# Performance work log

Measured on AMD Instinct MI355X. Metric: run time of the kernel, lower is better.

The kernel has to match this reference:

```python
import jax, jax.numpy as jnp
import numpy as np

N_NODES = 100000


def gcn_conv(x, edge_index, W, b):
    """PyG GCNConv: h = x @ W; out = D^-1/2 (A+I) D^-1/2 h + b."""
    n = x.shape[0]
    src, dst = edge_index[0], edge_index[1]
    loop = jnp.arange(n)
    src = jnp.concatenate([src, loop])  # add self-loops
    dst = jnp.concatenate([dst, loop])
    # degree at target nodes (unit edge weights)
    deg = jax.ops.segment_sum(jnp.ones(dst.shape[0], dtype=x.dtype), dst, num_segments=n)
    dinv = jnp.where(deg > 0, jax.lax.rsqrt(deg), 0.0)
    norm = dinv[src] * dinv[dst]  # [E+n]
    h = x @ W  # [n, out]
    msg = h[src] * norm[:, None]  # gather + scale
    out = jax.ops.segment_sum(msg, dst, num_segments=n)  # scatter-add
    return out + b


def setup_inputs() -> dict:
    key = jax.random.key(0)
    k1, k2, k3, k4, k5, k6 = jax.random.split(key, 6)
    E = 3200000
    x = jax.random.normal(k1, (N_NODES, 2), dtype=jnp.float32)
    edge_index = jax.random.randint(k2, (2, E), 0, N_NODES, dtype=jnp.int64)
    W1 = jax.random.normal(k3, (2, 16), dtype=jnp.float32) * 0.5
    b1 = jax.random.normal(k4, (16,), dtype=jnp.float32) * 0.1
    W2 = jax.random.normal(k5, (16, 2), dtype=jnp.float32) * 0.25
    b2 = jax.random.normal(k6, (2,), dtype=jnp.float32) * 0.1
    return {"x": x, "edge_index": edge_index, "W1": W1, "b1": b1, "W2": W2, "b2": b2}


def reference(x, edge_index, W1, b1, W2, b2):
    h = jax.nn.relu(gcn_conv(x, edge_index, W1, b1))
    # dropout is identity at inference
    out = gcn_conv(h, edge_index, W2, b2)
    return jax.nn.log_softmax(out, axis=1)
```

## Files before the change

kernel.cpp:

```cpp
#include <hip/hip_runtime.h>
#include <math.h>


constexpr int N = 100000;
constexpr int LOGB = 6;
constexpr int BNODES = 1 << LOGB;
constexpr int K = (N + BNODES - 1) / BNODES;
constexpr int KF = 49 * 32;
constexpr int CAPF = 2560;
constexpr int NC = 49;
constexpr int CAP1 = 68608;
constexpr int BSP = 512;
constexpr int ECHUNK = 8192;
constexpr int EPT = ECHUNK / BSP;
constexpr int MAXCH = 9;

__global__ __launch_bounds__(BSP) void k_pass1(const int* __restrict__ src,
                                               const int* __restrict__ dst, int E,
                                               int* __restrict__ gfill1,
                                               int* __restrict__ slotsC) {
    __shared__ int hist[NC];
    __shared__ int base[NC];
    int t = threadIdx.x;
    if (t < NC) hist[t] = 0;
    __syncthreads();
    int s[EPT], d[EPT];
    int ebase = blockIdx.x * ECHUNK + t * EPT;
#pragma unroll
    for (int k = 0; k < EPT / 4; k++) {
        int idx = ebase + 4 * k;
        if (idx + 3 < E) {
            *(int4*)(s + 4 * k) = *(const int4*)(src + idx);
            *(int4*)(d + 4 * k) = *(const int4*)(dst + idx);
        } else {
            for (int j = 0; j < 4; j++) {
                s[4 * k + j] = (idx + j < E) ? src[idx + j] : -1;
                d[4 * k + j] = (idx + j < E) ? dst[idx + j] : -1;
            }
        }
    }
#pragma unroll
    for (int k = 0; k < EPT; k++)
        if (d[k] >= 0) atomicAdd(&hist[d[k] >> 11], 1);
    __syncthreads();
    if (t < NC) {
        int c = hist[t];
        base[t] = c ? atomicAdd(&gfill1[t], c) : 0;
        hist[t] = 0;
    }
    __syncthreads();
#pragma unroll
    for (int k = 0; k < EPT; k++) {
        if (d[k] >= 0) {
            int bin = d[k] >> 11;
            int r = atomicAdd(&hist[bin], 1);
            int pos = base[bin] + r;
            if (pos < CAP1) slotsC[bin * CAP1 + pos] = (s[k] << 11) | (d[k] & 2047);
        }
    }
}

__global__ __launch_bounds__(BSP) void k_pass2(const int* __restrict__ gfill1,
                                               const int* __restrict__ slotsC,
                                               int* __restrict__ gfillF,
                                               int* __restrict__ slotsF) {
    __shared__ int hist[32];
    __shared__ int base[32];
    int c = blockIdx.x / MAXCH;
    int j = blockIdx.x % MAXCH;
    int fill = min(gfill1[c], CAP1);
    int e0 = j * ECHUNK;
    if (e0 >= fill) return;
    int e1 = min(fill, e0 + ECHUNK);
    int t = threadIdx.x;
    if (t < 32) hist[t] = 0;
    __syncthreads();
    const int* row = slotsC + c * CAP1;
    int v[EPT];
    int ebase = e0 + t * EPT;
#pragma unroll
    for (int k = 0; k < EPT / 4; k++) {
        int idx = ebase + 4 * k;
        if (idx + 3 < e1) {
            *(int4*)(v + 4 * k) = *(const int4*)(row + idx);
        } else {
            for (int jj = 0; jj < 4; jj++) v[4 * k + jj] = (idx + jj < e1) ? row[idx + jj] : -1;
        }
    }
#pragma unroll
    for (int k = 0; k < EPT; k++)
        if (v[k] >= 0) atomicAdd(&hist[(v[k] >> 6) & 31], 1);
    __syncthreads();
    if (t < 32) {
        int cc = hist[t];
        base[t] = cc ? atomicAdd(&gfillF[c * 32 + t], cc) : 0;
        hist[t] = 0;
    }
    __syncthreads();
#pragma unroll
    for (int k = 0; k < EPT; k++) {
        if (v[k] >= 0) {
            int b = (v[k] >> 6) & 31;
            int r = atomicAdd(&hist[b], 1);
            int pos = base[b] + r;
            if (pos < CAPF)
                slotsF[(c * 32 + b) * CAPF + pos] = ((v[k] >> 11) << 6) | (v[k] & 63);
        }
    }
}

__global__ __launch_bounds__(512) void k_degree(const int* __restrict__ gfillF,
                                                const int* __restrict__ slotsF,
                                                const float* __restrict__ x,
                                                float* __restrict__ dinv,
                                                float2* __restrict__ sx) {
    __shared__ int cnt[BNODES];
    int b = blockIdx.x, t = threadIdx.x;
    if (t < BNODES) cnt[t] = 0;
    __syncthreads();
    int count = min(gfillF[b], CAPF);
    const int* row = slotsF + b * CAPF;
    int nvec = count & ~3;
    for (int j = 4 * t; j < nvec; j += 4 * 512) {
        int4 p = *(const int4*)(row + j);
        atomicAdd(&cnt[p.x & (BNODES - 1)], 1);
        atomicAdd(&cnt[p.y & (BNODES - 1)], 1);
        atomicAdd(&cnt[p.z & (BNODES - 1)], 1);
        atomicAdd(&cnt[p.w & (BNODES - 1)], 1);
    }
    for (int j = nvec + t; j < count; j += 512) atomicAdd(&cnt[row[j] & (BNODES - 1)], 1);
    __syncthreads();
    if (t < BNODES) {
        int node = b * BNODES + t;
        if (node < N) {
            float di = rsqrtf((float)(cnt[t] + 1));
            dinv[node] = di;
            float2 xv = ((const float2*)x)[node];
            sx[node] = make_float2(xv.x * di, xv.y * di);
        }
    }
}

__global__ __launch_bounds__(512) void k_agg1(const int* __restrict__ gfillF,
                                              const int* __restrict__ slotsF,
                                              const float* __restrict__ dinv,
                                              const float2* __restrict__ sx,
                                              const float* __restrict__ W1,
                                              const float* __restrict__ b1,
                                              const float* __restrict__ W2,
                                              float2* __restrict__ sz) {
    __shared__ float accX[BNODES], accY[BNODES];
    __shared__ float sW1[32], sb1[16], sW2[32];
    int t = threadIdx.x;
    if (t < 32) sW1[t] = W1[t];
    if (t >= 32 && t < 48) sb1[t - 32] = b1[t - 32];
    if (t >= 48 && t < 80) sW2[t - 48] = W2[t - 48];
    if (t < BNODES) { accX[t] = 0.f; accY[t] = 0.f; }
    __syncthreads();
    int b = blockIdx.x;
    int count = min(gfillF[b], CAPF);
    const int* row = slotsF + b * CAPF;
    int nvec = count & ~3;
    for (int j = 4 * t; j < nvec; j += 4 * 512) {
        int4 p = *(const int4*)(row + j);
        float2 v0 = sx[p.x >> LOGB], v1 = sx[p.y >> LOGB];
        float2 v2 = sx[p.z >> LOGB], v3 = sx[p.w >> LOGB];
        atomicAdd(&accX[p.x & (BNODES - 1)], v0.x);
        atomicAdd(&accY[p.x & (BNODES - 1)], v0.y);
        atomicAdd(&accX[p.y & (BNODES - 1)], v1.x);
        atomicAdd(&accY[p.y & (BNODES - 1)], v1.y);
        atomicAdd(&accX[p.z & (BNODES - 1)], v2.x);
        atomicAdd(&accY[p.z & (BNODES - 1)], v2.y);
        atomicAdd(&accX[p.w & (BNODES - 1)], v3.x);
        atomicAdd(&accY[p.w & (BNODES - 1)], v3.y);
    }
    for (int j = nvec + t; j < count; j += 512) {
        int p = row[j];
        float2 v = sx[p >> LOGB];
        atomicAdd(&accX[p & (BNODES - 1)], v.x);
        atomicAdd(&accY[p & (BNODES - 1)], v.y);
    }
    __syncthreads();
    if (t < BNODES) {
        int node = b * BNODES + t;
        if (node < N) {
            float di = dinv[node];
            float2 sv = sx[node];
            float a0 = (accX[t] + sv.x) * di;
            float a1 = (accY[t] + sv.y) * di;
            float z0 = 0.f, z1 = 0.f;
#pragma unroll
            for (int k = 0; k < 16; k++) {
                float h = fmaf(a0, sW1[k], fmaf(a1, sW1[16 + k], sb1[k]));
                h = fmaxf(h, 0.f);
                z0 = fmaf(h, sW2[2 * k + 0], z0);
                z1 = fmaf(h, sW2[2 * k + 1], z1);
            }
            sz[node] = make_float2(z0 * di, z1 * di);
        }
    }
}

__global__ __launch_bounds__(512) void k_agg2(const int* __restrict__ gfillF,
                                              const int* __restrict__ slotsF,
                                              const float* __restrict__ dinv,
                                              const float2* __restrict__ sz,
                                              const float* __restrict__ b2,
                                              float2* __restrict__ out) {
    __shared__ float accX[BNODES], accY[BNODES];
    int b = blockIdx.x, t = threadIdx.x;
    if (t < BNODES) { accX[t] = 0.f; accY[t] = 0.f; }
    __syncthreads();
    int count = min(gfillF[b], CAPF);
    const int* row = slotsF + b * CAPF;
    int nvec = count & ~3;
    for (int j = 4 * t; j < nvec; j += 4 * 512) {
        int4 p = *(const int4*)(row + j);
        float2 v0 = sz[p.x >> LOGB], v1 = sz[p.y >> LOGB];
        float2 v2 = sz[p.z >> LOGB], v3 = sz[p.w >> LOGB];
        atomicAdd(&accX[p.x & (BNODES - 1)], v0.x);
        atomicAdd(&accY[p.x & (BNODES - 1)], v0.y);
        atomicAdd(&accX[p.y & (BNODES - 1)], v1.x);
        atomicAdd(&accY[p.y & (BNODES - 1)], v1.y);
        atomicAdd(&accX[p.z & (BNODES - 1)], v2.x);
        atomicAdd(&accY[p.z & (BNODES - 1)], v2.y);
        atomicAdd(&accX[p.w & (BNODES - 1)], v3.x);
        atomicAdd(&accY[p.w & (BNODES - 1)], v3.y);
    }
    for (int j = nvec + t; j < count; j += 512) {
        int p = row[j];
        float2 v = sz[p >> LOGB];
        atomicAdd(&accX[p & (BNODES - 1)], v.x);
        atomicAdd(&accY[p & (BNODES - 1)], v.y);
    }
    __syncthreads();
    if (t < BNODES) {
        int node = b * BNODES + t;
        if (node < N) {
            float di = dinv[node];
            float2 sv = sz[node];
            float v0 = fmaf(accX[t] + sv.x, di, b2[0]);
            float v1 = fmaf(accY[t] + sv.y, di, b2[1]);
            float m = fmaxf(v0, v1);
            float lse = m + logf(expf(v0 - m) + expf(v1 - m));
            out[node] = make_float2(v0 - lse, v1 - lse);
        }
    }
}

extern "C" void kernel_launch(void* const* d_in, const int* in_sizes, int n_in,
                              void* d_out, int out_size, void* d_ws, size_t ws_size,
                              hipStream_t stream) {
    const float* x  = (const float*)d_in[0];
    const int*   ei = (const int*)d_in[1];
    const float* W1 = (const float*)d_in[2];
    const float* b1 = (const float*)d_in[3];
    const float* W2 = (const float*)d_in[4];
    const float* b2 = (const float*)d_in[5];

    const int E = in_sizes[1] / 2;
    const int* src = ei;
    const int* dst = ei + E;
    const int GP = (E + ECHUNK - 1) / ECHUNK;

    char* ws = (char*)d_ws;
    size_t off = 0;
    auto alloc = [&](size_t bytes) {
        char* p = ws + off;
        off += (bytes + 511) & ~size_t(511);
        return p;
    };
    int*    fills  = (int*)alloc((NC + KF) * sizeof(int));
    float*  dinv   = (float*)alloc(N * sizeof(float));
    float2* sx     = (float2*)alloc(N * sizeof(float2));
    float2* sz     = (float2*)alloc(N * sizeof(float2));
    int*    slotsC = (int*)alloc((size_t)NC * CAP1 * sizeof(int));
    int*    slotsF = (int*)alloc((size_t)KF * CAPF * sizeof(int));
    int* gfill1 = fills;
    int* gfillF = fills + NC;

    hipMemsetAsync(fills, 0, (NC + KF) * sizeof(int), stream);

    k_pass1<<<GP, BSP, 0, stream>>>(src, dst, E, gfill1, slotsC);
    k_pass2<<<NC * MAXCH, BSP, 0, stream>>>(gfill1, slotsC, gfillF, slotsF);
    k_degree<<<K, 512, 0, stream>>>(gfillF, slotsF, x, dinv, sx);
    k_agg1<<<K, 512, 0, stream>>>(gfillF, slotsF, dinv, sx, W1, b1, W2, sz);
    k_agg2<<<K, 512, 0, stream>>>(gfillF, slotsF, dinv, sz, b2, (float2*)d_out);
}
```

Measured before the change: 203.2 us.

## Fuse degree counting into bucket pass and batch aggregation gathers

Degree counting moves into the second bucketing pass: each block keeps a 2048-bin shared histogram and writes partial counts, which a small per-node kernel sums to produce dinv and the scaled features. This removes the separate k_degree pass over the fine-grained slot array. The aggregation kernels now use 256 threads, each loading up to 12 packed edges up front and issuing all feature gathers before the shared atomics, to raise memory-level parallelism. In exchange, the early return for empty chunks is gone, adding shared-memory init and partial-count writes for every block. The fixed 12-per-thread scheme also assumes bucket counts stay within the 2560 capacity.

```diff
diff --git a/kernel.cpp b/kernel.cpp
--- a/kernel.cpp
+++ b/kernel.cpp
@@ -63,18 +63,20 @@
 __global__ __launch_bounds__(BSP) void k_pass2(const int* __restrict__ gfill1,
                                                const int* __restrict__ slotsC,
                                                int* __restrict__ gfillF,
-                                               int* __restrict__ slotsF) {
+                                               int* __restrict__ slotsF,
+                                               int* __restrict__ cntp) {
     __shared__ int hist[32];
     __shared__ int base[32];
+    __shared__ int cnt[2048];
     int c = blockIdx.x / MAXCH;
     int j = blockIdx.x % MAXCH;
+    int t = threadIdx.x;
+    if (t < 32) hist[t] = 0;
+    for (int i = t; i < 2048; i += BSP) cnt[i] = 0;
+    __syncthreads();
     int fill = min(gfill1[c], CAP1);
     int e0 = j * ECHUNK;
-    if (e0 >= fill) return;
     int e1 = min(fill, e0 + ECHUNK);
-    int t = threadIdx.x;
-    if (t < 32) hist[t] = 0;
-    __syncthreads();
     const int* row = slotsC + c * CAP1;
     int v[EPT];
     int ebase = e0 + t * EPT;
@@ -88,8 +90,12 @@
         }
     }
 #pragma unroll
-    for (int k = 0; k < EPT; k++)
-        if (v[k] >= 0) atomicAdd(&hist[(v[k] >> 6) & 31], 1);
+    for (int k = 0; k < EPT; k++) {
+        if (v[k] >= 0) {
+            atomicAdd(&hist[(v[k] >> 6) & 31], 1);
+            atomicAdd(&cnt[v[k] & 2047], 1);
+        }
+    }
     __syncthreads();
     if (t < 32) {
         int cc = hist[t];
@@ -107,41 +113,36 @@
                 slotsF[(c * 32 + b) * CAPF + pos] = ((v[k] >> 11) << 6) | (v[k] & 63);
         }
     }
-}
-
-__global__ __launch_bounds__(512) void k_degree(const int* __restrict__ gfillF,
-                                                const int* __restrict__ slotsF,
-                                                const float* __restrict__ x,
-                                                float* __restrict__ dinv,
-                                                float2* __restrict__ sx) {
-    __shared__ int cnt[BNODES];
-    int b = blockIdx.x, t = threadIdx.x;
-    if (t < BNODES) cnt[t] = 0;
-    __syncthreads();
-    int count = min(gfillF[b], CAPF);
-    const int* row = slotsF + b * CAPF;
-    int nvec = count & ~3;
-    for (int j = 4 * t; j < nvec; j += 4 * 512) {
-        int4 p = *(const int4*)(row + j);
-        atomicAdd(&cnt[p.x & (BNODES - 1)], 1);
-        atomicAdd(&cnt[p.y & (BNODES - 1)], 1);
-        atomicAdd(&cnt[p.z & (BNODES - 1)], 1);
-        atomicAdd(&cnt[p.w & (BNODES - 1)], 1);
-    }
-    for (int j = nvec + t; j < count; j += 512) atomicAdd(&cnt[row[j] & (BNODES - 1)], 1);
-    __syncthreads();
-    if (t < BNODES) {
-        int node = b * BNODES + t;
-        if (node < N) {
-            float di = rsqrtf((float)(cnt[t] + 1));
-            dinv[node] = di;
-            float2 xv = ((const float2*)x)[node];
-            sx[node] = make_float2(xv.x * di, xv.y * di);
-        }
-    }
-}
-
-__global__ __launch_bounds__(512) void k_agg1(const int* __restrict__ gfillF,
+    int* out = cntp + (size_t)blockIdx.x * 2048;
+    *(int4*)(out + 4 * t) = *(const int4*)(cnt + 4 * t);
+}
+
+__global__ void k_node1(const int* __restrict__ cntp, const float* __restrict__ x,
+                        float* __restrict__ dinv, float2* __restrict__ sx) {
+    int i = blockIdx.x * blockDim.x + threadIdx.x;
+    if (i >= N) return;
+    int c = i >> 11, l = i & 2047;
+    const int* p = cntp + (size_t)c * MAXCH * 2048 + l;
+    int s = 0;
+#pragma unroll
+    for (int j = 0; j < MAXCH; j++) s += p[j * 2048];
+    float di = rsqrtf((float)(s + 1));
+    dinv[i] = di;
+    float2 xv = ((const float2*)x)[i];
+    sx[i] = make_float2(xv.x * di, xv.y * di);
+}
+
+__device__ __forceinline__ int4 gload(const int* __restrict__ row, int j, int cnt) {
+    if (j + 3 < cnt) return *(const int4*)(row + j);
+    int4 p = make_int4(-1, -1, -1, -1);
+    if (j + 0 < cnt) p.x = row[j + 0];
+    if (j + 1 < cnt) p.y = row[j + 1];
+    if (j + 2 < cnt) p.z = row[j + 2];
+    if (j + 3 < cnt) p.w = row[j + 3];
+    return p;
+}
+
+__global__ __launch_bounds__(256) void k_agg1(const int* __restrict__ gfillF,
                                               const int* __restrict__ slotsF,
                                               const float* __restrict__ dinv,
                                               const float2* __restrict__ sx,
@@ -159,26 +160,28 @@
     __syncthreads();
     int b = blockIdx.x;
     int count = min(gfillF[b], CAPF);
-    const int* row = slotsF + b * CAPF;
-    int nvec = count & ~3;
-    for (int j = 4 * t; j < nvec; j += 4 * 512) {
-        int4 p = *(const int4*)(row + j);
-        float2 v0 = sx[p.x >> LOGB], v1 = sx[p.y >> LOGB];
-        float2 v2 = sx[p.z >> LOGB], v3 = sx[p.w >> LOGB];
-        atomicAdd(&accX[p.x & (BNODES - 1)], v0.x);
-        atomicAdd(&accY[p.x & (BNODES - 1)], v0.y);
-        atomicAdd(&accX[p.y & (BNODES - 1)], v1.x);
-        atomicAdd(&accY[p.y & (BNODES - 1)], v1.y);
-        atomicAdd(&accX[p.z & (BNODES - 1)], v2.x);
-        atomicAdd(&accY[p.z & (BNODES - 1)], v2.y);
-        atomicAdd(&accX[p.w & (BNODES - 1)], v3.x);
-        atomicAdd(&accY[p.w & (BNODES - 1)], v3.y);
-    }
-    for (int j = nvec + t; j < count; j += 512) {
-        int p = row[j];
-        float2 v = sx[p >> LOGB];
-        atomicAdd(&accX[p & (BNODES - 1)], v.x);
-        atomicAdd(&accY[p & (BNODES - 1)], v.y);
+    const int* row = slotsF + (size_t)b * CAPF;
+    int pk[12];
+    {
+        int4 p0 = gload(row, 4 * t, count);
+        int4 p1 = gload(row, 4 * t + 1024, count);
+        int4 p2 = gload(row, 4 * t + 2048, count);
+        pk[0] = p0.x; pk[1] = p0.y; pk[2] = p0.z; pk[3] = p0.w;
+        pk[4] = p1.x; pk[5] = p1.y; pk[6] = p1.z; pk[7] = p1.w;
+        pk[8] = p2.x; pk[9] = p2.y; pk[10] = p2.z; pk[11] = p2.w;
+    }
+    float2 vv[12];
+#pragma unroll
+    for (int m = 0; m < 12; m++) {
+        int idx = (pk[m] >= 0) ? (pk[m] >> LOGB) : 0;
+        vv[m] = sx[idx];
+    }
+#pragma unroll
+    for (int m = 0; m < 12; m++) {
+        if (pk[m] >= 0) {
+            atomicAdd(&accX[pk[m] & (BNODES - 1)], vv[m].x);
+            atomicAdd(&accY[pk[m] & (BNODES - 1)], vv[m].y);
+        }
     }
     __syncthreads();
     if (t < BNODES) {
@@ -201,7 +204,7 @@
     }
 }
 
-__global__ __launch_bounds__(512) void k_agg2(const int* __restrict__ gfillF,
+__global__ __launch_bounds__(256) void k_agg2(const int* __restrict__ gfillF,
                                               const int* __restrict__ slotsF,
                                               const float* __restrict__ dinv,
                                               const float2* __restrict__ sz,
@@ -212,26 +215,28 @@
     if (t < BNODES) { accX[t] = 0.f; accY[t] = 0.f; }
     __syncthreads();
     int count = min(gfillF[b], CAPF);
-    const int* row = slotsF + b * CAPF;
-    int nvec = count & ~3;
-    for (int j = 4 * t; j < nvec; j += 4 * 512) {
-        int4 p = *(const int4*)(row + j);
-        float2 v0 = sz[p.x >> LOGB], v1 = sz[p.y >> LOGB];
-        float2 v2 = sz[p.z >> LOGB], v3 = sz[p.w >> LOGB];
-        atomicAdd(&accX[p.x & (BNODES - 1)], v0.x);
-        atomicAdd(&accY[p.x & (BNODES - 1)], v0.y);
-        atomicAdd(&accX[p.y & (BNODES - 1)], v1.x);
-        atomicAdd(&accY[p.y & (BNODES - 1)], v1.y);
-        atomicAdd(&accX[p.z & (BNODES - 1)], v2.x);
-        atomicAdd(&accY[p.z & (BNODES - 1)], v2.y);
-        atomicAdd(&accX[p.w & (BNODES - 1)], v3.x);
-        atomicAdd(&accY[p.w & (BNODES - 1)], v3.y);
-    }
-    for (int j = nvec + t; j < count; j += 512) {
-        int p = row[j];
-        float2 v = sz[p >> LOGB];
-        atomicAdd(&accX[p & (BNODES - 1)], v.x);
-        atomicAdd(&accY[p & (BNODES - 1)], v.y);
+    const int* row = slotsF + (size_t)b * CAPF;
+    int pk[12];
+    {
+        int4 p0 = gload(row, 4 * t, count);
+        int4 p1 = gload(row, 4 * t + 1024, count);
+        int4 p2 = gload(row, 4 * t + 2048, count);
+        pk[0] = p0.x; pk[1] = p0.y; pk[2] = p0.z; pk[3] = p0.w;
+        pk[4] = p1.x; pk[5] = p1.y; pk[6] = p1.z; pk[7] = p1.w;
+        pk[8] = p2.x; pk[9] = p2.y; pk[10] = p2.z; pk[11] = p2.w;
+    }
+    float2 vv[12];
+#pragma unroll
+    for (int m = 0; m < 12; m++) {
+        int idx = (pk[m] >= 0) ? (pk[m] >> LOGB) : 0;
+        vv[m] = sz[idx];
+    }
+#pragma unroll
+    for (int m = 0; m < 12; m++) {
+        if (pk[m] >= 0) {
+            atomicAdd(&accX[pk[m] & (BNODES - 1)], vv[m].x);
+            atomicAdd(&accY[pk[m] & (BNODES - 1)], vv[m].y);
+        }
     }
     __syncthreads();
     if (t < BNODES) {
@@ -276,14 +281,15 @@
     float2* sz     = (float2*)alloc(N * sizeof(float2));
     int*    slotsC = (int*)alloc((size_t)NC * CAP1 * sizeof(int));
     int*    slotsF = (int*)alloc((size_t)KF * CAPF * sizeof(int));
+    int*    cntp   = (int*)alloc((size_t)NC * MAXCH * 2048 * sizeof(int));
     int* gfill1 = fills;
     int* gfillF = fills + NC;
 
     hipMemsetAsync(fills, 0, (NC + KF) * sizeof(int), stream);
 
     k_pass1<<<GP, BSP, 0, stream>>>(src, dst, E, gfill1, slotsC);
-    k_pass2<<<NC * MAXCH, BSP, 0, stream>>>(gfill1, slotsC, gfillF, slotsF);
-    k_degree<<<K, 512, 0, stream>>>(gfillF, slotsF, x, dinv, sx);
-    k_agg1<<<K, 512, 0, stream>>>(gfillF, slotsF, dinv, sx, W1, b1, W2, sz);
-    k_agg2<<<K, 512, 0, stream>>>(gfillF, slotsF, dinv, sz, b2, (float2*)d_out);
-}
+    k_pass2<<<NC * MAXCH, BSP, 0, stream>>>(gfill1, slotsC, gfillF, slotsF, cntp);
+    k_node1<<<(N + 255) / 256, 256, 0, stream>>>(cntp, x, dinv, sx);
+    k_agg1<<<K, 256, 0, stream>>>(gfillF, slotsF, dinv, sx, W1, b1, W2, sz);
+    k_agg2<<<K, 256, 0, stream>>>(gfillF, slotsF, dinv, sz, b2, (float2*)d_out);
+}
```

Result: no change. 203.5 us (+0.2%).

## Replace LDS atomic aggregation with per-lane match-and-accumulate over each bucket

Applied to the files above, without the earlier changes.

The degree and both aggregation kernels move to 256-thread blocks. Each of the 4 waves scans a quarter of the 64-node bucket's edge list, and every lane adds only the edges whose destination matches its lane id. Per-wave partial sums are combined through shared memory, which removes LDS atomics and makes the summation order deterministic. The cost is that every lane walks all edges in its quarter, so per-lane ALU work and the serial chain of dependent gathers grow about 64-fold. k_pass2 also drops its early return for empty chunks.

```diff
diff --git a/kernel.cpp b/kernel.cpp
--- a/kernel.cpp
+++ b/kernel.cpp
@@ -3,17 +3,18 @@
 
 
 constexpr int N = 100000;
-constexpr int LOGB = 6;
-constexpr int BNODES = 1 << LOGB;
-constexpr int K = (N + BNODES - 1) / BNODES;
-constexpr int KF = 49 * 32;
+constexpr int CLOG = 11;
+constexpr int CN = 1 << CLOG;
+constexpr int NC = 49;
+constexpr int KF = NC * 32;
+constexpr int K = (N + 63) / 64;
+constexpr int CAP1 = 68608;
 constexpr int CAPF = 2560;
-constexpr int NC = 49;
-constexpr int CAP1 = 68608;
 constexpr int BSP = 512;
 constexpr int ECHUNK = 8192;
 constexpr int EPT = ECHUNK / BSP;
 constexpr int MAXCH = 9;
+constexpr int WCH = CAPF / 4;
 
 __global__ __launch_bounds__(BSP) void k_pass1(const int* __restrict__ src,
                                                const int* __restrict__ dst, int E,
@@ -41,7 +42,7 @@
     }
 #pragma unroll
     for (int k = 0; k < EPT; k++)
-        if (d[k] >= 0) atomicAdd(&hist[d[k] >> 11], 1);
+        if (d[k] >= 0) atomicAdd(&hist[d[k] >> CLOG], 1);
     __syncthreads();
     if (t < NC) {
         int c = hist[t];
@@ -52,10 +53,10 @@
 #pragma unroll
     for (int k = 0; k < EPT; k++) {
         if (d[k] >= 0) {
-            int bin = d[k] >> 11;
+            int bin = d[k] >> CLOG;
             int r = atomicAdd(&hist[bin], 1);
             int pos = base[bin] + r;
-            if (pos < CAP1) slotsC[bin * CAP1 + pos] = (s[k] << 11) | (d[k] & 2047);
+            if (pos < CAP1) slotsC[bin * CAP1 + pos] = (s[k] << CLOG) | (d[k] & (CN - 1));
         }
     }
 }
@@ -68,13 +69,12 @@
     __shared__ int base[32];
     int c = blockIdx.x / MAXCH;
     int j = blockIdx.x % MAXCH;
+    int t = threadIdx.x;
+    if (t < 32) hist[t] = 0;
+    __syncthreads();
     int fill = min(gfill1[c], CAP1);
     int e0 = j * ECHUNK;
-    if (e0 >= fill) return;
     int e1 = min(fill, e0 + ECHUNK);
-    int t = threadIdx.x;
-    if (t < 32) hist[t] = 0;
-    __syncthreads();
     const int* row = slotsC + c * CAP1;
     int v[EPT];
     int ebase = e0 + t * EPT;
@@ -100,40 +100,42 @@
 #pragma unroll
     for (int k = 0; k < EPT; k++) {
         if (v[k] >= 0) {
-            int b = (v[k] >> 6) & 31;
-            int r = atomicAdd(&hist[b], 1);
-            int pos = base[b] + r;
+            int fb = (v[k] >> 6) & 31;
+            int r = atomicAdd(&hist[fb], 1);
+            int pos = base[fb] + r;
             if (pos < CAPF)
-                slotsF[(c * 32 + b) * CAPF + pos] = ((v[k] >> 11) << 6) | (v[k] & 63);
-        }
-    }
-}
-
-__global__ __launch_bounds__(512) void k_degree(const int* __restrict__ gfillF,
-                                                const int* __restrict__ slotsF,
-                                                const float* __restrict__ x,
-                                                float* __restrict__ dinv,
-                                                float2* __restrict__ sx) {
-    __shared__ int cnt[BNODES];
-    int b = blockIdx.x, t = threadIdx.x;
-    if (t < BNODES) cnt[t] = 0;
-    __syncthreads();
+                slotsF[(size_t)(c * 32 + fb) * CAPF + pos] = ((v[k] >> CLOG) << 6) | (v[k] & 63);
+        }
+    }
+}
+
+__global__ __launch_bounds__(256) void k_deg(const int* __restrict__ gfillF,
+                                             const int* __restrict__ slotsF,
+                                             const float* __restrict__ x,
+                                             float* __restrict__ dinv,
+                                             float2* __restrict__ sx) {
+    __shared__ int pdeg[4][64];
+    int b = blockIdx.x, t = threadIdx.x, w = t >> 6, lane = t & 63;
     int count = min(gfillF[b], CAPF);
-    const int* row = slotsF + b * CAPF;
-    int nvec = count & ~3;
-    for (int j = 4 * t; j < nvec; j += 4 * 512) {
-        int4 p = *(const int4*)(row + j);
-        atomicAdd(&cnt[p.x & (BNODES - 1)], 1);
-        atomicAdd(&cnt[p.y & (BNODES - 1)], 1);
-        atomicAdd(&cnt[p.z & (BNODES - 1)], 1);
-        atomicAdd(&cnt[p.w & (BNODES - 1)], 1);
-    }
-    for (int j = nvec + t; j < count; j += 512) atomicAdd(&cnt[row[j] & (BNODES - 1)], 1);
-    __syncthreads();
-    if (t < BNODES) {
-        int node = b * BNODES + t;
+    const int* row = slotsF + (size_t)b * CAPF;
+    int j0 = w * WCH, j1 = min(count, j0 + WCH);
+    int deg = 0;
+    int j = j0;
+    for (; j + 8 <= j1; j += 8) {
+        int e[8];
+#pragma unroll
+        for (int k = 0; k < 8; k++) e[k] = row[j + k];
+#pragma unroll
+        for (int k = 0; k < 8; k++) deg += ((e[k] & 63) == lane) ? 1 : 0;
+    }
+    for (; j < j1; j++) deg += ((row[j] & 63) == lane) ? 1 : 0;
+    pdeg[w][lane] = deg;
+    __syncthreads();
+    if (t < 64) {
+        int node = b * 64 + t;
         if (node < N) {
-            float di = rsqrtf((float)(cnt[t] + 1));
+            int d = pdeg[0][t] + pdeg[1][t] + pdeg[2][t] + pdeg[3][t];
+            float di = rsqrtf((float)(d + 1));
             dinv[node] = di;
             float2 xv = ((const float2*)x)[node];
             sx[node] = make_float2(xv.x * di, xv.y * di);
@@ -141,7 +143,7 @@
     }
 }
 
-__global__ __launch_bounds__(512) void k_agg1(const int* __restrict__ gfillF,
+__global__ __launch_bounds__(256) void k_agg1(const int* __restrict__ gfillF,
                                               const int* __restrict__ slotsF,
                                               const float* __restrict__ dinv,
                                               const float2* __restrict__ sx,
@@ -149,49 +151,53 @@
                                               const float* __restrict__ b1,
                                               const float* __restrict__ W2,
                                               float2* __restrict__ sz) {
-    __shared__ float accX[BNODES], accY[BNODES];
+    __shared__ float pax[4][64], pay[4][64];
     __shared__ float sW1[32], sb1[16], sW2[32];
     int t = threadIdx.x;
     if (t < 32) sW1[t] = W1[t];
     if (t >= 32 && t < 48) sb1[t - 32] = b1[t - 32];
     if (t >= 48 && t < 80) sW2[t - 48] = W2[t - 48];
-    if (t < BNODES) { accX[t] = 0.f; accY[t] = 0.f; }
-    __syncthreads();
-    int b = blockIdx.x;
+    int b = blockIdx.x, w = t >> 6, lane = t & 63;
     int count = min(gfillF[b], CAPF);
-    const int* row = slotsF + b * CAPF;
-    int nvec = count & ~3;
-    for (int j = 4 * t; j < nvec; j += 4 * 512) {
-        int4 p = *(const int4*)(row + j);
-        float2 v0 = sx[p.x >> LOGB], v1 = sx[p.y >> LOGB];
-        float2 v2 = sx[p.z >> LOGB], v3 = sx[p.w >> LOGB];
-        atomicAdd(&accX[p.x & (BNODES - 1)], v0.x);
-        atomicAdd(&accY[p.x & (BNODES - 1)], v0.y);
-        atomicAdd(&accX[p.y & (BNODES - 1)], v1.x);
-        atomicAdd(&accY[p.y & (BNODES - 1)], v1.y);
-        atomicAdd(&accX[p.z & (BNODES - 1)], v2.x);
-        atomicAdd(&accY[p.z & (BNODES - 1)], v2.y);
-        atomicAdd(&accX[p.w & (BNODES - 1)], v3.x);
-        atomicAdd(&accY[p.w & (BNODES - 1)], v3.y);
-    }
-    for (int j = nvec + t; j < count; j += 512) {
-        int p = row[j];
-        float2 v = sx[p >> LOGB];
-        atomicAdd(&accX[p & (BNODES - 1)], v.x);
-        atomicAdd(&accY[p & (BNODES - 1)], v.y);
-    }
-    __syncthreads();
-    if (t < BNODES) {
-        int node = b * BNODES + t;
+    const int* row = slotsF + (size_t)b * CAPF;
+    int j0 = w * WCH, j1 = min(count, j0 + WCH);
+    float a0 = 0.f, a1 = 0.f;
+    int j = j0;
+    for (; j + 8 <= j1; j += 8) {
+        int e[8];
+#pragma unroll
+        for (int k = 0; k < 8; k++) e[k] = row[j + k];
+        float2 v[8];
+#pragma unroll
+        for (int k = 0; k < 8; k++) v[k] = sx[e[k] >> 6];
+#pragma unroll
+        for (int k = 0; k < 8; k++) {
+            bool m = (e[k] & 63) == lane;
+            a0 += m ? v[k].x : 0.f;
+            a1 += m ? v[k].y : 0.f;
+        }
+    }
+    for (; j < j1; j++) {
+        int e = row[j];
+        float2 v = sx[e >> 6];
+        bool m = (e & 63) == lane;
+        a0 += m ? v.x : 0.f;
+        a1 += m ? v.y : 0.f;
+    }
+    pax[w][lane] = a0;
+    pay[w][lane] = a1;
+    __syncthreads();
+    if (t < 64) {
+        int node = b * 64 + t;
         if (node < N) {
             float di = dinv[node];
             float2 sv = sx[node];
-            float a0 = (accX[t] + sv.x) * di;
-            float a1 = (accY[t] + sv.y) * di;
+            float A0 = (pax[0][t] + pax[1][t] + pax[2][t] + pax[3][t] + sv.x) * di;
+            float A1 = (pay[0][t] + pay[1][t] + pay[2][t] + pay[3][t] + sv.y) * di;
             float z0 = 0.f, z1 = 0.f;
 #pragma unroll
             for (int k = 0; k < 16; k++) {
-                float h = fmaf(a0, sW1[k], fmaf(a1, sW1[16 + k], sb1[k]));
+                float h = fmaf(A0, sW1[k], fmaf(A1, sW1[16 + k], sb1[k]));
                 h = fmaxf(h, 0.f);
                 z0 = fmaf(h, sW2[2 * k + 0], z0);
                 z1 = fmaf(h, sW2[2 * k + 1], z1);
@@ -201,46 +207,50 @@
     }
 }
 
-__global__ __launch_bounds__(512) void k_agg2(const int* __restrict__ gfillF,
+__global__ __launch_bounds__(256) void k_agg2(const int* __restrict__ gfillF,
                                               const int* __restrict__ slotsF,
                                               const float* __restrict__ dinv,
                                               const float2* __restrict__ sz,
                                               const float* __restrict__ b2,
                                               float2* __restrict__ out) {
-    __shared__ float accX[BNODES], accY[BNODES];
-    int b = blockIdx.x, t = threadIdx.x;
-    if (t < BNODES) { accX[t] = 0.f; accY[t] = 0.f; }
-    __syncthreads();
+    __shared__ float pax[4][64], pay[4][64];
+    int b = blockIdx.x, t = threadIdx.x, w = t >> 6, lane = t & 63;
     int count = min(gfillF[b], CAPF);
-    const int* row = slotsF + b * CAPF;
-    int nvec = count & ~3;
-    for (int j = 4 * t; j < nvec; j += 4 * 512) {
-        int4 p = *(const int4*)(row + j);
-        float2 v0 = sz[p.x >> LOGB], v1 = sz[p.y >> LOGB];
-        float2 v2 = sz[p.z >> LOGB], v3 = sz[p.w >> LOGB];
-        atomicAdd(&accX[p.x & (BNODES - 1)], v0.x);
-        atomicAdd(&accY[p.x & (BNODES - 1)], v0.y);
-        atomicAdd(&accX[p.y & (BNODES - 1)], v1.x);
-        atomicAdd(&accY[p.y & (BNODES - 1)], v1.y);
-        atomicAdd(&accX[p.z & (BNODES - 1)], v2.x);
-        atomicAdd(&accY[p.z & (BNODES - 1)], v2.y);
-        atomicAdd(&accX[p.w & (BNODES - 1)], v3.x);
-        atomicAdd(&accY[p.w & (BNODES - 1)], v3.y);
-    }
-    for (int j = nvec + t; j < count; j += 512) {
-        int p = row[j];
-        float2 v = sz[p >> LOGB];
-        atomicAdd(&accX[p & (BNODES - 1)], v.x);
-        atomicAdd(&accY[p & (BNODES - 1)], v.y);
-    }
-    __syncthreads();
-    if (t < BNODES) {
-        int node = b * BNODES + t;
+    const int* row = slotsF + (size_t)b * CAPF;
+    int j0 = w * WCH, j1 = min(count, j0 + WCH);
+    float a0 = 0.f, a1 = 0.f;
+    int j = j0;
+    for (; j + 8 <= j1; j += 8) {
+        int e[8];
+#pragma unroll
+        for (int k = 0; k < 8; k++) e[k] = row[j + k];
+        float2 v[8];
+#pragma unroll
+        for (int k = 0; k < 8; k++) v[k] = sz[e[k] >> 6];
+#pragma unroll
+        for (int k = 0; k < 8; k++) {
+            bool m = (e[k] & 63) == lane;
+            a0 += m ? v[k].x : 0.f;
+            a1 += m ? v[k].y : 0.f;
+        }
+    }
+    for (; j < j1; j++) {
+        int e = row[j];
+        float2 v = sz[e >> 6];
+        bool m = (e & 63) == lane;
+        a0 += m ? v.x : 0.f;
+        a1 += m ? v.y : 0.f;
+    }
+    pax[w][lane] = a0;
+    pay[w][lane] = a1;
+    __syncthreads();
+    if (t < 64) {
+        int node = b * 64 + t;
         if (node < N) {
             float di = dinv[node];
             float2 sv = sz[node];
-            float v0 = fmaf(accX[t] + sv.x, di, b2[0]);
-            float v1 = fmaf(accY[t] + sv.y, di, b2[1]);
+            float v0 = fmaf(pax[0][t] + pax[1][t] + pax[2][t] + pax[3][t] + sv.x, di, b2[0]);
+            float v1 = fmaf(pay[0][t] + pay[1][t] + pay[2][t] + pay[3][t] + sv.y, di, b2[1]);
             float m = fmaxf(v0, v1);
             float lse = m + logf(expf(v0 - m) + expf(v1 - m));
             out[node] = make_float2(v0 - lse, v1 - lse);
@@ -283,7 +293,7 @@
 
     k_pass1<<<GP, BSP, 0, stream>>>(src, dst, E, gfill1, slotsC);
     k_pass2<<<NC * MAXCH, BSP, 0, stream>>>(gfill1, slotsC, gfillF, slotsF);
-    k_degree<<<K, 512, 0, stream>>>(gfillF, slotsF, x, dinv, sx);
-    k_agg1<<<K, 512, 0, stream>>>(gfillF, slotsF, dinv, sx, W1, b1, W2, sz);
-    k_agg2<<<K, 512, 0, stream>>>(gfillF, slotsF, dinv, sz, b2, (float2*)d_out);
-}
+    k_deg<<<K, 256, 0, stream>>>(gfillF, slotsF, x, dinv, sx);
+    k_agg1<<<K, 256, 0, stream>>>(gfillF, slotsF, dinv, sx, W1, b1, W2, sz);
+    k_agg2<<<K, 256, 0, stream>>>(gfillF, slotsF, dinv, sz, b2, (float2*)d_out);
+}
```

Result: slower. 435.6 us (+114.4%).
